# Kernel optimization log

Hardware: AMD Instinct MI355X
Metric: run time of the kernel (lower is better)

Reference implementation:

```python
import jax, jax.numpy as jnp
import numpy as np

EMBED = 1024  # point_net_embedding_dim
H1, H2 = 512, 256  # head_hidden_layer_sizes


def _init(key, shape, fan_in):
    return jax.random.normal(key, shape, dtype=jnp.float32) / jnp.sqrt(jnp.float32(fan_in))


def setup_inputs() -> dict:
    key = jax.random.key(0)
    ks = jax.random.split(key, 13)
    B, N = 256, 1024
    x = jax.random.normal(ks[0], (B, N, 3), dtype=jnp.float32)
    # PointNet shared per-point MLP: 3 -> 64 -> 128 -> EMBED (ReLU), max-pool over points
    W1 = _init(ks[1], (3, 64), 3);        b1 = jnp.zeros((64,), jnp.float32)
    W2 = _init(ks[2], (64, 128), 64);     b2 = jnp.zeros((128,), jnp.float32)
    W3 = _init(ks[3], (128, EMBED), 128); b3 = jnp.zeros((EMBED,), jnp.float32)
    # Head MLP: EMBED -> 512 -> 256 -> 9 (no final activation)
    Wh1 = _init(ks[4], (EMBED, H1), EMBED); bh1 = jnp.zeros((H1,), jnp.float32)
    Wh2 = _init(ks[5], (H1, H2), H1);       bh2 = jnp.zeros((H2,), jnp.float32)
    Wh3 = _init(ks[6], (H2, 9), H2);        bh3 = jnp.zeros((9,), jnp.float32)
    return {"x": x, "W1": W1, "b1": b1, "W2": W2, "b2": b2, "W3": W3, "b3": b3,
            "Wh1": Wh1, "bh1": bh1, "Wh2": Wh2, "bh2": bh2, "Wh3": Wh3, "bh3": bh3}


def svd_projection(M):
    # Project raw 3x3 matrices onto SO(3): R = U diag(1,1,det(U V^T)) V^T
    U, S, Vh = jnp.linalg.svd(M, full_matrices=False)
    det = jnp.linalg.det(jnp.einsum('...ij,...jk->...ik', U, Vh))
    d = jnp.stack([jnp.ones_like(det), jnp.ones_like(det), det], axis=-1)  # [..., 3]
    return jnp.einsum('...ij,...j,...jk->...ik', U, d, Vh)


def reference(x, W1, b1, W2, b2, W3, b3, Wh1, bh1, Wh2, bh2, Wh3, bh3):
    # Shared per-point MLP (ReLU), final_activation=ReLU, then max-pool over points
    h = jax.nn.relu(x @ W1 + b1)          # [B, N, 64]
    h = jax.nn.relu(h @ W2 + b2)          # [B, N, 128]
    h = jax.nn.relu(h @ W3 + b3)          # [B, N, EMBED]
    g = jnp.max(h, axis=-2)               # [B, EMBED] global feature
    # Head MLP -> raw 3x3
    z = jax.nn.relu(g @ Wh1 + bh1)
    z = jax.nn.relu(z @ Wh2 + bh2)
    raw = (z @ Wh3 + bh3).reshape(*x.shape[:-2], 3, 3)
    return svd_projection(raw)
```

## Files before the change

kernel.cpp:

```cpp
#include <hip/hip_runtime.h>
#include <math.h>

typedef _Float16 f16;
typedef _Float16 f16x8 __attribute__((ext_vector_type(8)));
typedef float f32x4 __attribute__((ext_vector_type(4)));

__global__ __launch_bounds__(256) void prep_weights(
    const float* __restrict__ W1, const float* __restrict__ b1,
    const float* __restrict__ W2, const float* __restrict__ W3,
    f16* __restrict__ W2t, f16* __restrict__ W3t, float* __restrict__ wpk)
{
    int idx = blockIdx.x * 256 + threadIdx.x;
    int stride = gridDim.x * 256;
    for (int i = idx; i < 1024 * 128; i += stride) {
        int c = i >> 7, k = i & 127;
        W3t[i] = (f16)W3[k * 1024 + c];
    }
    for (int i = idx; i < 128 * 64; i += stride) {
        int c = i >> 6, k = i & 63;
        W2t[i] = (f16)W2[k * 128 + c];
    }
    if (idx < 256) {
        int k = idx >> 2, c = idx & 3;
        wpk[idx] = (c < 3) ? W1[c * 64 + k] : b1[k];
    }
}

__global__ __launch_bounds__(512, 2) void pointnet_fused(
    const float* __restrict__ x,
    const float* __restrict__ wpk,
    const f16* __restrict__ W2t,
    const float* __restrict__ b2,
    const f16* __restrict__ W3t,
    const float* __restrict__ b3,
    float* __restrict__ g)
{
    __shared__ float xs[1024 * 3];
    __shared__ __align__(16) float wls[288];
    __shared__ float b2s[128];
    __shared__ __align__(16) f16 h2s[2][128 * 136];

    int b = blockIdx.x;
    int tid = threadIdx.x;
    int lane = tid & 63, w = tid >> 6;
    int lrow = lane & 15, quad = lane >> 4;
    int wr2 = w & 3, wc2 = w >> 2;

    f16x8 bf3[8][4];
    {
        const f16* base = W3t + (size_t)(w * 128 + lrow) * 128 + quad * 8;
#pragma unroll
        for (int ct = 0; ct < 8; ct++)
#pragma unroll
            for (int kc = 0; kc < 4; kc++)
                bf3[ct][kc] = *(const f16x8*)(base + ct * 16 * 128 + kc * 32);
    }
    f16x8 bf2[4][2];
    {
        const f16* base = W2t + (size_t)(wc2 * 64 + lrow) * 64 + quad * 8;
#pragma unroll
        for (int ct = 0; ct < 4; ct++)
#pragma unroll
            for (int kc2 = 0; kc2 < 2; kc2++)
                bf2[ct][kc2] = *(const f16x8*)(base + ct * 16 * 64 + kc2 * 32);
    }

    {
        const float* xb = x + (size_t)b * 3072;
        for (int i = tid; i < 3072; i += 512) xs[i] = xb[i];
        if (tid < 256) {
            int k = tid >> 2, c = tid & 3;
            wls[(k + (k >> 3)) * 4 + c] = wpk[tid];
        }
        if (tid >= 256 && tid < 384) b2s[tid - 256] = b2[tid - 256];
    }
    __syncthreads();

    const f32x4 z4 = {0.f, 0.f, 0.f, 0.f};
    float cmax[8];
#pragma unroll
    for (int ct = 0; ct < 8; ct++) cmax[ct] = -3.0e38f;

    auto phaseA = [&](int chunk) {
        f16* hb = h2s[chunk & 1];
        int p0 = chunk * 128 + wr2 * 32 + lrow;
        float x00 = xs[p0 * 3], x01 = xs[p0 * 3 + 1], x02 = xs[p0 * 3 + 2];
        int p1 = p0 + 16;
        float x10 = xs[p1 * 3], x11 = xs[p1 * 3 + 1], x12 = xs[p1 * 3 + 2];
        f32x4 acc2[2][4];
#pragma unroll
        for (int kc2 = 0; kc2 < 2; kc2++) {
            f16x8 af2[2];
#pragma unroll
            for (int j = 0; j < 8; j++) {
                int k = kc2 * 32 + quad * 8 + j;
                f32x4 wv = *(const f32x4*)&wls[(k + (k >> 3)) * 4];
                float v0 = fmaf(x02, wv[2], fmaf(x01, wv[1], fmaf(x00, wv[0], wv[3])));
                float v1 = fmaf(x12, wv[2], fmaf(x11, wv[1], fmaf(x10, wv[0], wv[3])));
                af2[0][j] = (f16)fmaxf(v0, 0.f);
                af2[1][j] = (f16)fmaxf(v1, 0.f);
            }
#pragma unroll
            for (int rt = 0; rt < 2; rt++)
#pragma unroll
                for (int ct = 0; ct < 4; ct++)
                    acc2[rt][ct] = __builtin_amdgcn_mfma_f32_16x16x32_f16(
                        af2[rt], bf2[ct][kc2], kc2 ? acc2[rt][ct] : z4, 0, 0, 0);
        }
#pragma unroll
        for (int rt = 0; rt < 2; rt++)
#pragma unroll
            for (int ct = 0; ct < 4; ct++) {
                int col = wc2 * 64 + ct * 16 + lrow;
                float bb = b2s[col];
                int rowb = wr2 * 32 + rt * 16 + quad * 4;
#pragma unroll
                for (int r = 0; r < 4; r++)
                    hb[(rowb + r) * 136 + col] = (f16)fmaxf(acc2[rt][ct][r] + bb, 0.f);
            }
    };

    auto phaseB = [&](int chunk) {
        const f16* hb = h2s[chunk & 1];
#pragma unroll
        for (int rt = 0; rt < 8; rt++) {
            f32x4 acc[8];
#pragma unroll
            for (int kc = 0; kc < 4; kc++) {
                f16x8 af = *(const f16x8*)(hb + (rt * 16 + lrow) * 136 + kc * 32 + quad * 8);
#pragma unroll
                for (int ct = 0; ct < 8; ct++)
                    acc[ct] = __builtin_amdgcn_mfma_f32_16x16x32_f16(
                        af, bf3[ct][kc], kc ? acc[ct] : z4, 0, 0, 0);
            }
#pragma unroll
            for (int ct = 0; ct < 8; ct++) {
                float m01 = fmaxf(acc[ct][0], acc[ct][1]);
                float m23 = fmaxf(acc[ct][2], acc[ct][3]);
                cmax[ct] = fmaxf(cmax[ct], fmaxf(m01, m23));
            }
        }
    };

    phaseA(0);
    __syncthreads();
#pragma unroll 1
    for (int c = 0; c < 7; c++) {
        phaseA(c + 1);
        phaseB(c);
        __syncthreads();
    }
    phaseB(7);

#pragma unroll
    for (int ct = 0; ct < 8; ct++) {
        cmax[ct] = fmaxf(cmax[ct], __shfl_xor(cmax[ct], 16, 64));
        cmax[ct] = fmaxf(cmax[ct], __shfl_xor(cmax[ct], 32, 64));
    }
    if (quad == 0) {
#pragma unroll
        for (int ct = 0; ct < 8; ct++) {
            int cg = w * 128 + ct * 16 + lrow;
            g[(size_t)b * 1024 + cg] = fmaxf(cmax[ct] + b3[cg], 0.f);
        }
    }
}

__global__ __launch_bounds__(256) void head_l1(
    const float* __restrict__ g, const float* __restrict__ Wh1,
    float* __restrict__ zp1)
{
    __shared__ float gs4[4][256];
    int cb = blockIdx.x, bb = blockIdx.y, kc = blockIdx.z;
    int tid = threadIdx.x;
    int b0 = bb * 4;
    int kbase = kc * 256;
#pragma unroll
    for (int j = 0; j < 4; j++) {
        int i = tid + j * 256;
        gs4[i >> 8][i & 255] = g[(size_t)(b0 + (i >> 8)) * 1024 + kbase + (i & 255)];
    }
    __syncthreads();

    int c = cb * 256 + tid;
    float acc[4] = {0.f, 0.f, 0.f, 0.f};
#pragma unroll 1
    for (int k = 0; k < 256; k += 8) {
        float w[8];
#pragma unroll
        for (int j = 0; j < 8; j++) w[j] = Wh1[(size_t)(kbase + k + j) * 512 + c];
#pragma unroll
        for (int r = 0; r < 4; r++) {
            float4 a = *(const float4*)&gs4[r][k];
            float4 bq = *(const float4*)&gs4[r][k + 4];
            acc[r] = fmaf(a.x, w[0], acc[r]);
            acc[r] = fmaf(a.y, w[1], acc[r]);
            acc[r] = fmaf(a.z, w[2], acc[r]);
            acc[r] = fmaf(a.w, w[3], acc[r]);
            acc[r] = fmaf(bq.x, w[4], acc[r]);
            acc[r] = fmaf(bq.y, w[5], acc[r]);
            acc[r] = fmaf(bq.z, w[6], acc[r]);
            acc[r] = fmaf(bq.w, w[7], acc[r]);
        }
    }
#pragma unroll
    for (int r = 0; r < 4; r++)
        zp1[((size_t)kc * 256 + b0 + r) * 512 + c] = acc[r];
}

__global__ __launch_bounds__(256) void head_l2(
    const float* __restrict__ zp1, const float* __restrict__ bh1,
    const float* __restrict__ Wh2, float* __restrict__ zp2)
{
    __shared__ float z1s[2][128];
    int bb = blockIdx.x, kc2 = blockIdx.y;
    int tid = threadIdx.x;
    int b0 = bb * 2;
    int kb = kc2 * 128;
    {
        int row = tid >> 7, kk = tid & 127;
        int col = kb + kk;
        float v = bh1[col];
#pragma unroll
        for (int j = 0; j < 4; j++)
            v += zp1[((size_t)j * 256 + b0 + row) * 512 + col];
        z1s[row][kk] = fmaxf(v, 0.f);
    }
    __syncthreads();

    int c = tid;
    float acc0 = 0.f, acc1 = 0.f;
#pragma unroll 1
    for (int k = 0; k < 128; k += 8) {
        float w[8];
#pragma unroll
        for (int j = 0; j < 8; j++) w[j] = Wh2[(size_t)(kb + k + j) * 256 + c];
        float4 a0 = *(const float4*)&z1s[0][k];
        float4 a1 = *(const float4*)&z1s[0][k + 4];
        float4 d0 = *(const float4*)&z1s[1][k];
        float4 d1 = *(const float4*)&z1s[1][k + 4];
        acc0 = fmaf(a0.x, w[0], acc0);  acc1 = fmaf(d0.x, w[0], acc1);
        acc0 = fmaf(a0.y, w[1], acc0);  acc1 = fmaf(d0.y, w[1], acc1);
        acc0 = fmaf(a0.z, w[2], acc0);  acc1 = fmaf(d0.z, w[2], acc1);
        acc0 = fmaf(a0.w, w[3], acc0);  acc1 = fmaf(d0.w, w[3], acc1);
        acc0 = fmaf(a1.x, w[4], acc0);  acc1 = fmaf(d1.x, w[4], acc1);
        acc0 = fmaf(a1.y, w[5], acc0);  acc1 = fmaf(d1.y, w[5], acc1);
        acc0 = fmaf(a1.z, w[6], acc0);  acc1 = fmaf(d1.z, w[6], acc1);
        acc0 = fmaf(a1.w, w[7], acc0);  acc1 = fmaf(d1.w, w[7], acc1);
    }
    zp2[((size_t)kc2 * 256 + b0    ) * 256 + c] = acc0;
    zp2[((size_t)kc2 * 256 + b0 + 1) * 256 + c] = acc1;
}

__device__ inline void jrot(double S[3][3], double V[3][3], int p, int q)
{
    double apq = S[p][q];
    if (fabs(apq) < 1e-36) return;
    double tau = (S[q][q] - S[p][p]) / (2.0 * apq);
    double t = (tau >= 0.0 ? 1.0 : -1.0) / (fabs(tau) + sqrt(1.0 + tau * tau));
    double c = 1.0 / sqrt(1.0 + t * t);
    double s = t * c;
    for (int k = 0; k < 3; k++) {
        double skp = S[k][p], skq = S[k][q];
        S[k][p] = c * skp - s * skq;  S[k][q] = s * skp + c * skq;
    }
    for (int k = 0; k < 3; k++) {
        double spk = S[p][k], sqk = S[q][k];
        S[p][k] = c * spk - s * sqk;  S[q][k] = s * spk + c * sqk;
    }
    for (int k = 0; k < 3; k++) {
        double vkp = V[k][p], vkq = V[k][q];
        V[k][p] = c * vkp - s * vkq;  V[k][q] = s * vkp + c * vkq;
    }
}

__device__ void svd_so3(const float* Mf, float* Rout)
{
    double M[3][3], S[3][3], V[3][3];
    for (int i = 0; i < 3; i++)
        for (int j = 0; j < 3; j++) M[i][j] = (double)Mf[3 * i + j];
    for (int i = 0; i < 3; i++)
        for (int j = 0; j < 3; j++)
            S[i][j] = M[0][i] * M[0][j] + M[1][i] * M[1][j] + M[2][i] * M[2][j];
    for (int i = 0; i < 3; i++)
        for (int j = 0; j < 3; j++) V[i][j] = (i == j) ? 1.0 : 0.0;
    for (int it = 0; it < 10; it++) {
        jrot(S, V, 0, 1); jrot(S, V, 0, 2); jrot(S, V, 1, 2);
    }
    double lam[3] = {S[0][0], S[1][1], S[2][2]};
    int i0 = 0, i1 = 1, i2 = 2, tt;
    if (lam[i0] < lam[i1]) { tt = i0; i0 = i1; i1 = tt; }
    if (lam[i0] < lam[i2]) { tt = i0; i0 = i2; i2 = tt; }
    if (lam[i1] < lam[i2]) { tt = i1; i1 = i2; i2 = tt; }
    double v0[3], v1[3], v2[3];
    for (int k = 0; k < 3; k++) { v0[k] = V[k][i0]; v1[k] = V[k][i1]; v2[k] = V[k][i2]; }
    double u1[3], u2[3], u3[3];
    for (int i = 0; i < 3; i++) u1[i] = M[i][0] * v0[0] + M[i][1] * v0[1] + M[i][2] * v0[2];
    double n1 = sqrt(u1[0] * u1[0] + u1[1] * u1[1] + u1[2] * u1[2]) + 1e-300;
    for (int i = 0; i < 3; i++) u1[i] /= n1;
    for (int i = 0; i < 3; i++) u2[i] = M[i][0] * v1[0] + M[i][1] * v1[1] + M[i][2] * v1[2];
    double d12 = u1[0] * u2[0] + u1[1] * u2[1] + u1[2] * u2[2];
    for (int i = 0; i < 3; i++) u2[i] -= d12 * u1[i];
    double n2 = sqrt(u2[0] * u2[0] + u2[1] * u2[1] + u2[2] * u2[2]) + 1e-300;
    for (int i = 0; i < 3; i++) u2[i] /= n2;
    u3[0] = u1[1] * u2[2] - u1[2] * u2[1];
    u3[1] = u1[2] * u2[0] - u1[0] * u2[2];
    u3[2] = u1[0] * u2[1] - u1[1] * u2[0];
    double c12x = v1[1] * v2[2] - v1[2] * v2[1];
    double c12y = v1[2] * v2[0] - v1[0] * v2[2];
    double c12z = v1[0] * v2[1] - v1[1] * v2[0];
    double detV = v0[0] * c12x + v0[1] * c12y + v0[2] * c12z;
    for (int i = 0; i < 3; i++)
        for (int j = 0; j < 3; j++)
            Rout[3 * i + j] = (float)(u1[i] * v0[j] + u2[i] * v1[j] + detV * u3[i] * v2[j]);
}

__global__ __launch_bounds__(128) void head_l3_svd(
    const float* __restrict__ zp2, const float* __restrict__ bh2,
    const float* __restrict__ Wh3, const float* __restrict__ bh3,
    float* __restrict__ out)
{
    __shared__ float z2s[8][256];
    __shared__ float wh3s[2304];
    __shared__ float raws[8][12];
    int b0 = blockIdx.x * 8;
    int tid = threadIdx.x;

    for (int i = tid; i < 2304; i += 128) wh3s[i] = Wh3[i];
    for (int i = tid; i < 8 * 256; i += 128) {
        int row = i >> 8, kk = i & 255;
        float v = bh2[kk];
#pragma unroll
        for (int j = 0; j < 4; j++)
            v += zp2[((size_t)j * 256 + b0 + row) * 256 + kk];
        z2s[row][kk] = fmaxf(v, 0.f);
    }
    __syncthreads();

    if (tid < 72) {
        int r = tid / 9, c = tid % 9;
        float acc = bh3[c];
#pragma unroll 8
        for (int k = 0; k < 256; k++) acc = fmaf(z2s[r][k], wh3s[k * 9 + c], acc);
        raws[r][c] = acc;
    }
    __syncthreads();

    if (tid < 8) svd_so3(&raws[tid][0], out + (size_t)(b0 + tid) * 9);
}

extern "C" void kernel_launch(void* const* d_in, const int* in_sizes, int n_in,
                              void* d_out, int out_size, void* d_ws, size_t ws_size,
                              hipStream_t stream)
{
    const float* x   = (const float*)d_in[0];
    const float* W1  = (const float*)d_in[1];
    const float* b1  = (const float*)d_in[2];
    const float* W2  = (const float*)d_in[3];
    const float* b2  = (const float*)d_in[4];
    const float* W3  = (const float*)d_in[5];
    const float* b3  = (const float*)d_in[6];
    const float* Wh1 = (const float*)d_in[7];
    const float* bh1 = (const float*)d_in[8];
    const float* Wh2 = (const float*)d_in[9];
    const float* bh2 = (const float*)d_in[10];
    const float* Wh3 = (const float*)d_in[11];
    const float* bh3 = (const float*)d_in[12];
    float* out = (float*)d_out;

    char* ws = (char*)d_ws;
    f16*   W2t = (f16*)ws;
    f16*   W3t = (f16*)(ws + 65536);
    float* wpk = (float*)(ws + 524288);
    float* g   = (float*)(ws + 1048576);
    float* zp1 = (float*)(ws + 2097152);
    float* zp2 = (float*)(ws + 4194304);

    prep_weights<<<128, 256, 0, stream>>>(W1, b1, W2, W3, W2t, W3t, wpk);
    pointnet_fused<<<256, 512, 0, stream>>>(x, wpk, W2t, b2, W3t, b3, g);
    dim3 gridH1(2, 64, 4);
    head_l1<<<gridH1, 256, 0, stream>>>(g, Wh1, zp1);
    dim3 gridH2(128, 4);
    head_l2<<<gridH2, 256, 0, stream>>>(zp1, bh1, Wh2, zp2);
    head_l3_svd<<<32, 128, 0, stream>>>(zp2, bh2, Wh3, bh3, out);
}
```

Before: 177.6 us.

## Pad h2 LDS stride, raise wave priority in MFMA phase, drop head_l1 staging

Changes the padded row stride of the shared h2 buffer from 136 to 140 halves to alter the LDS bank mapping for the phaseB fragment loads. Wraps the MFMA-heavy phaseB in s_setprio(1)/s_setprio(0) so waves in the matrix phase get issue priority over waves in phaseA. In head_l1, removes the shared-memory staging of g and the barrier, and reads g directly from global memory (uniform scalar loads), relying on caches. The 140 stride makes rows only 8-byte aligned, so the 16-byte f16x8 LDS reads may be split into narrower accesses.

```diff
diff --git a/kernel.cpp b/kernel.cpp
--- a/kernel.cpp
+++ b/kernel.cpp
@@ -4,6 +4,8 @@
 typedef _Float16 f16;
 typedef _Float16 f16x8 __attribute__((ext_vector_type(8)));
 typedef float f32x4 __attribute__((ext_vector_type(4)));
+
+#define H2_STRIDE 140
 
 __global__ __launch_bounds__(256) void prep_weights(
     const float* __restrict__ W1, const float* __restrict__ b1,
@@ -38,7 +40,7 @@
     __shared__ float xs[1024 * 3];
     __shared__ __align__(16) float wls[288];
     __shared__ float b2s[128];
-    __shared__ __align__(16) f16 h2s[2][128 * 136];
+    __shared__ __align__(16) f16 h2s[2][128 * H2_STRIDE];
 
     int b = blockIdx.x;
     int tid = threadIdx.x;
@@ -116,18 +118,19 @@
                 int rowb = wr2 * 32 + rt * 16 + quad * 4;
 #pragma unroll
                 for (int r = 0; r < 4; r++)
-                    hb[(rowb + r) * 136 + col] = (f16)fmaxf(acc2[rt][ct][r] + bb, 0.f);
+                    hb[(rowb + r) * H2_STRIDE + col] = (f16)fmaxf(acc2[rt][ct][r] + bb, 0.f);
             }
     };
 
     auto phaseB = [&](int chunk) {
         const f16* hb = h2s[chunk & 1];
+        __builtin_amdgcn_s_setprio(1);
 #pragma unroll
         for (int rt = 0; rt < 8; rt++) {
             f32x4 acc[8];
 #pragma unroll
             for (int kc = 0; kc < 4; kc++) {
-                f16x8 af = *(const f16x8*)(hb + (rt * 16 + lrow) * 136 + kc * 32 + quad * 8);
+                f16x8 af = *(const f16x8*)(hb + (rt * 16 + lrow) * H2_STRIDE + kc * 32 + quad * 8);
 #pragma unroll
                 for (int ct = 0; ct < 8; ct++)
                     acc[ct] = __builtin_amdgcn_mfma_f32_16x16x32_f16(
@@ -140,6 +143,7 @@
                 cmax[ct] = fmaxf(cmax[ct], fmaxf(m01, m23));
             }
         }
+        __builtin_amdgcn_s_setprio(0);
     };
 
     phaseA(0);
@@ -170,19 +174,13 @@
     const float* __restrict__ g, const float* __restrict__ Wh1,
     float* __restrict__ zp1)
 {
-    __shared__ float gs4[4][256];
     int cb = blockIdx.x, bb = blockIdx.y, kc = blockIdx.z;
     int tid = threadIdx.x;
     int b0 = bb * 4;
     int kbase = kc * 256;
-#pragma unroll
-    for (int j = 0; j < 4; j++) {
-        int i = tid + j * 256;
-        gs4[i >> 8][i & 255] = g[(size_t)(b0 + (i >> 8)) * 1024 + kbase + (i & 255)];
-    }
-    __syncthreads();
-
     int c = cb * 256 + tid;
+    const float* gb = g + (size_t)b0 * 1024 + kbase;
+
     float acc[4] = {0.f, 0.f, 0.f, 0.f};
 #pragma unroll 1
     for (int k = 0; k < 256; k += 8) {
@@ -190,18 +188,10 @@
 #pragma unroll
         for (int j = 0; j < 8; j++) w[j] = Wh1[(size_t)(kbase + k + j) * 512 + c];
 #pragma unroll
-        for (int r = 0; r < 4; r++) {
-            float4 a = *(const float4*)&gs4[r][k];
-            float4 bq = *(const float4*)&gs4[r][k + 4];
-            acc[r] = fmaf(a.x, w[0], acc[r]);
-            acc[r] = fmaf(a.y, w[1], acc[r]);
-            acc[r] = fmaf(a.z, w[2], acc[r]);
-            acc[r] = fmaf(a.w, w[3], acc[r]);
-            acc[r] = fmaf(bq.x, w[4], acc[r]);
-            acc[r] = fmaf(bq.y, w[5], acc[r]);
-            acc[r] = fmaf(bq.z, w[6], acc[r]);
-            acc[r] = fmaf(bq.w, w[7], acc[r]);
-        }
+        for (int r = 0; r < 4; r++)
+#pragma unroll
+            for (int j = 0; j < 8; j++)
+                acc[r] = fmaf(gb[r * 1024 + k + j], w[j], acc[r]);
     }
 #pragma unroll
     for (int r = 0; r < 4; r++)
```

New measurement: 202.8 us. 14.2% more time.
